# Kernel optimization log

Hardware: AMD Instinct MI355X
Metric: run time of the kernel (lower is better)

The kernel has to match this reference:

```python
import jax, jax.numpy as jnp
import numpy as np

INPUT_DIM = 1024
HIDDEN_DIM = 2048
NUM_BLOCKS = 8
BLOCK_SIZE = HIDDEN_DIM // NUM_BLOCKS
BATCH = 2048


def setup_inputs() -> dict:
    key = jax.random.key(0)
    ks = jax.random.split(key, 6)
    # PyTorch GRUCell init: uniform(-1/sqrt(hidden_size), 1/sqrt(hidden_size))
    bound = 1.0 / np.sqrt(BLOCK_SIZE)
    u = lambda k, shape: jax.random.uniform(k, shape, jnp.float32, -bound, bound)
    return {
        "input": jax.random.normal(ks[0], (BATCH, INPUT_DIM), jnp.float32),
        "hidden": jax.random.normal(ks[1], (BATCH, HIDDEN_DIM), jnp.float32),
        # stacked per-block GRUCell params (block-diagonal structure)
        "W_ih": u(ks[2], (NUM_BLOCKS, 3 * BLOCK_SIZE, INPUT_DIM)),
        "W_hh": u(ks[3], (NUM_BLOCKS, 3 * BLOCK_SIZE, BLOCK_SIZE)),
        "b_ih": u(ks[4], (NUM_BLOCKS, 3 * BLOCK_SIZE)),
        "b_hh": u(ks[5], (NUM_BLOCKS, 3 * BLOCK_SIZE)),
    }


def reference(input, hidden, W_ih, W_hh, b_ih, b_hh):
    B = input.shape[0]
    nb, g3, bs = W_hh.shape  # [num_blocks, 3*block_size, block_size]
    hb = hidden.reshape(B, nb, bs)                      # [B, nb, bs]
    # input-to-gate and hidden-to-gate projections, batched over blocks
    gi = jnp.einsum("bi,ngi->bng", input, W_ih) + b_ih  # [B, nb, 3*bs]
    gh = jnp.einsum("bns,ngs->bng", hb, W_hh) + b_hh    # [B, nb, 3*bs]
    i_r, i_z, i_n = jnp.split(gi, 3, axis=-1)
    h_r, h_z, h_n = jnp.split(gh, 3, axis=-1)
    r = jax.nn.sigmoid(i_r + h_r)
    z = jax.nn.sigmoid(i_z + h_z)
    n = jnp.tanh(i_n + r * h_n)
    new_h = (1.0 - z) * n + z * hb                      # [B, nb, bs]
    return new_h.reshape(B, nb * bs)
```

## Files before the change

### kernel.cpp

```cpp
#include <hip/hip_runtime.h>
#include <hip/hip_bf16.h>
#include <type_traits>

typedef __attribute__((ext_vector_type(4))) float f32x4;
typedef __attribute__((ext_vector_type(8))) short bf16x8;

template <int V> using ic = std::integral_constant<int, V>;

static constexpr int B_   = 2048;
static constexpr int IN_  = 1024;
static constexpr int HID_ = 2048;
static constexpr int NB_  = 8;
static constexpr int BS_  = 256;
static constexpr int G3_  = 768;

__device__ __forceinline__ unsigned cvtpk(float lo, float hi) {
  unsigned r;
  asm("v_cvt_pk_bf16_f32 %0, %1, %2" : "=v"(r) : "v"(lo), "v"(hi));
  return r;
}

__global__ __launch_bounds__(256, 2) void gru_mfma(
    const float* __restrict__ xf,
    const float* __restrict__ hf,
    const float* __restrict__ Wih,
    const float* __restrict__ Whh,
    const float* __restrict__ b_ih,
    const float* __restrict__ b_hh,
    float* __restrict__ out)
{
  __shared__ __align__(16) char lds[2][40960];

  const int t    = threadIdx.x;
  const int lane = t & 63;
  const int wid  = t >> 6;
  const int wm   = wid >> 1;
  const int wn   = wid & 1;

  const int bid = blockIdx.x;
  const int swz = (bid & 7) * 64 + (bid >> 3);
  const int mrow0 = (swz & 15) * 128;
  const int ct    = swz >> 4;
  const int n     = ct >> 2;
  const int s0    = (ct & 3) * 64;

  int arow[4], acol[4];
#pragma unroll
  for (int p = 0; p < 4; ++p) {
    int op = p * 4096 + t * 16;
    int ol = op ^ (((op >> 7) & 7) << 4);
    arow[p] = ol >> 7;
    acol[p] = (ol & 127) >> 1;
  }
  int wgrow[6], wcol[6];
#pragma unroll
  for (int q = 0; q < 6; ++q) {
    int op = q * 4096 + t * 16;
    int ol = op ^ (((op >> 7) & 7) << 4);
    int wr = ol >> 7;
    wgrow[q] = n * G3_ + (wr >> 6) * BS_ + s0 + (wr & 63);
    wcol[q]  = (ol & 127) >> 1;
  }

  f32x4 acc[4][4][2] = {};
  float4 st[4][2];

  auto issueA = [&](int t2) {
#pragma unroll
    for (int p = 0; p < 4; ++p) {
      const float* src = (t2 < 16)
        ? xf + (size_t)(mrow0 + arow[p]) * IN_  + t2 * 64 + acol[p]
        : hf + (size_t)(mrow0 + arow[p]) * HID_ + n * BS_ + (t2 - 16) * 64 + acol[p];
      st[p][0] = *reinterpret_cast<const float4*>(src);
      st[p][1] = *reinterpret_cast<const float4*>(src + 4);
    }
  };
  auto issueW = [&](int t2, int q0) {
#pragma unroll
    for (int j = 0; j < 3; ++j) {
      const int q = q0 + j;
      const float* src = (t2 < 16)
        ? Wih + (size_t)wgrow[q] * IN_ + t2 * 64 + wcol[q]
        : Whh + (size_t)wgrow[q] * BS_ + (t2 - 16) * 64 + wcol[q];
      st[j][0] = *reinterpret_cast<const float4*>(src);
      st[j][1] = *reinterpret_cast<const float4*>(src + 4);
    }
  };
  auto pack8 = [&](const float4& a, const float4& b) {
    union { unsigned u[4]; bf16x8 v; } r;
    r.u[0] = cvtpk(a.x, a.y); r.u[1] = cvtpk(a.z, a.w);
    r.u[2] = cvtpk(b.x, b.y); r.u[3] = cvtpk(b.z, b.w);
    return r.v;
  };
  auto writeA = [&](char* buf) {
#pragma unroll
    for (int p = 0; p < 4; ++p)
      *reinterpret_cast<bf16x8*>(buf + p * 4096 + t * 16) = pack8(st[p][0], st[p][1]);
  };
  auto writeW = [&](char* buf, int q0) {
#pragma unroll
    for (int j = 0; j < 3; ++j)
      *reinterpret_cast<bf16x8*>(buf + 16384 + (q0 + j) * 4096 + t * 16) = pack8(st[j][0], st[j][1]);
  };

  auto loadA = [&](const char* buf, bf16x8 (&af)[2][4]) {
#pragma unroll
    for (int ksub = 0; ksub < 2; ++ksub)
#pragma unroll
      for (int mi = 0; mi < 4; ++mi) {
        int ar  = wm * 64 + mi * 16 + (lane & 15);
        int off = ar * 128 + ksub * 64 + ((lane >> 4) * 16);
        off ^= (ar & 7) << 4;
        af[ksub][mi] = *reinterpret_cast<const bf16x8*>(buf + off);
      }
  };
  auto loadW = [&](const char* buf, int g, bf16x8 (&wf)[2][2]) {
#pragma unroll
    for (int ksub = 0; ksub < 2; ++ksub)
#pragma unroll
      for (int ni = 0; ni < 2; ++ni) {
        int wr  = g * 64 + wn * 32 + ni * 16 + (lane & 15);
        int off = wr * 128 + ksub * 64 + ((lane >> 4) * 16);
        off ^= (wr & 7) << 4;
        wf[ksub][ni] = *reinterpret_cast<const bf16x8*>(buf + 16384 + off);
      }
  };
  auto mfmaSet = [&](auto setc, bf16x8 (&af)[2][4], bf16x8 (&wf)[2][2]) {
    constexpr int set = decltype(setc)::value;
    __builtin_amdgcn_s_setprio(1);
#pragma unroll
    for (int ksub = 0; ksub < 2; ++ksub)
#pragma unroll
      for (int mi = 0; mi < 4; ++mi)
#pragma unroll
        for (int ni = 0; ni < 2; ++ni)
          acc[set][mi][ni] = __builtin_amdgcn_mfma_f32_16x16x32_bf16(
              af[ksub][mi], wf[ksub][ni], acc[set][mi][ni], 0, 0, 0);
    __builtin_amdgcn_s_setprio(0);
  };

  issueA(0);
  writeA((char*)lds[0]);
  issueW(0, 0);
  writeW((char*)lds[0], 0);
  issueW(0, 3);
  writeW((char*)lds[0], 3);
  __syncthreads();

#pragma unroll
  for (int tt = 0; tt < 20; ++tt) {
    char* cur = (char*)lds[tt & 1];
    char* oth = (char*)lds[(tt & 1) ^ 1];
    bf16x8 af[2][4], wf[2][2];

    if (tt < 19) issueA(tt + 1);
    __builtin_amdgcn_sched_barrier(0);
    loadA(cur, af);
    loadW(cur, 0, wf);
    mfmaSet(ic<0>{}, af, wf);
    __builtin_amdgcn_sched_barrier(0);
    if (tt < 19) { writeA(oth); issueW(tt + 1, 0); }
    __builtin_amdgcn_sched_barrier(0);
    loadW(cur, 1, wf);
    mfmaSet(ic<1>{}, af, wf);
    __builtin_amdgcn_sched_barrier(0);
    if (tt < 19) { writeW(oth, 0); issueW(tt + 1, 3); }
    __builtin_amdgcn_sched_barrier(0);
    loadW(cur, 2, wf);
    if (tt < 16) mfmaSet(ic<2>{}, af, wf);
    else         mfmaSet(ic<3>{}, af, wf);
    __builtin_amdgcn_sched_barrier(0);
    if (tt < 19) writeW(oth, 3);
    __syncthreads();
  }

#pragma unroll
  for (int ni = 0; ni < 2; ++ni) {
    int scol = s0 + wn * 32 + ni * 16 + (lane & 15);
    float br_i = b_ih[n * G3_ + 0 * BS_ + scol];
    float bz_i = b_ih[n * G3_ + 1 * BS_ + scol];
    float bn_i = b_ih[n * G3_ + 2 * BS_ + scol];
    float br_h = b_hh[n * G3_ + 0 * BS_ + scol];
    float bz_h = b_hh[n * G3_ + 1 * BS_ + scol];
    float bn_h = b_hh[n * G3_ + 2 * BS_ + scol];
    int gcol = n * BS_ + scol;
#pragma unroll
    for (int mi = 0; mi < 4; ++mi) {
#pragma unroll
      for (int i = 0; i < 4; ++i) {
        int row = mrow0 + wm * 64 + mi * 16 + (lane >> 4) * 4 + i;
        float hprev = hf[(size_t)row * HID_ + gcol];
        float rr = acc[0][mi][ni][i] + br_i + br_h;
        float zz = acc[1][mi][ni][i] + bz_i + bz_h;
        float r  = 1.f / (1.f + __expf(-rr));
        float z  = 1.f / (1.f + __expf(-zz));
        float ng = tanhf(acc[2][mi][ni][i] + bn_i + r * (acc[3][mi][ni][i] + bn_h));
        out[(size_t)row * HID_ + gcol] = (1.f - z) * ng + z * hprev;
      }
    }
  }
}

extern "C" void kernel_launch(void* const* d_in, const int* in_sizes, int n_in,
                              void* d_out, int out_size, void* d_ws, size_t ws_size,
                              hipStream_t stream) {
  const float* x   = (const float*)d_in[0];
  const float* h   = (const float*)d_in[1];
  const float* Wih = (const float*)d_in[2];
  const float* Whh = (const float*)d_in[3];
  const float* bih = (const float*)d_in[4];
  const float* bhh = (const float*)d_in[5];
  float* out = (float*)d_out;
  (void)d_ws; (void)ws_size;

  gru_mfma<<<512, 256, 0, stream>>>(x, h, Wih, Whh, bih, bhh, out);
}
```

Baseline: 53.73 us.

## Halve K-tile to 32 and issue all next-tile loads before compute

Halves the K step per iteration from 64 to 32, so LDS per buffer drops from 40KB to 20KB and the loop runs 40 iterations instead of 20. All global loads for the next tile (A and the three W gates) are now issued together before compute, and their LDS writes happen after the MFMAs. Loads are no longer staggered between gate MFMA sets, and the LDS swizzle is changed to a 4-way XOR for 64-byte rows. The smaller LDS footprint could allow more blocks per CU, but doubling the number of iterations also doubles the barriers, and each MFMA phase is shorter for hiding latency.

```diff
diff --git a/kernel.cpp b/kernel.cpp
--- a/kernel.cpp
+++ b/kernel.cpp
@@ -29,7 +29,7 @@
     const float* __restrict__ b_hh,
     float* __restrict__ out)
 {
-  __shared__ __align__(16) char lds[2][40960];
+  __shared__ __align__(16) char lds[2][20480];
 
   const int t    = threadIdx.x;
   const int lane = t & 63;
@@ -44,46 +44,44 @@
   const int n     = ct >> 2;
   const int s0    = (ct & 3) * 64;
 
-  int arow[4], acol[4];
+  int arow[2], acolE[2];
 #pragma unroll
-  for (int p = 0; p < 4; ++p) {
+  for (int p = 0; p < 2; ++p) {
     int op = p * 4096 + t * 16;
-    int ol = op ^ (((op >> 7) & 7) << 4);
-    arow[p] = ol >> 7;
-    acol[p] = (ol & 127) >> 1;
+    int ol = op ^ (((op >> 6) & 3) << 4);
+    arow[p]  = ol >> 6;
+    acolE[p] = (ol & 63) >> 1;
   }
-  int wgrow[6], wcol[6];
+  int wgrow[3], wcolE[3];
 #pragma unroll
-  for (int q = 0; q < 6; ++q) {
+  for (int q = 0; q < 3; ++q) {
     int op = q * 4096 + t * 16;
-    int ol = op ^ (((op >> 7) & 7) << 4);
-    int wr = ol >> 7;
-    wgrow[q] = n * G3_ + (wr >> 6) * BS_ + s0 + (wr & 63);
-    wcol[q]  = (ol & 127) >> 1;
+    int ol = op ^ (((op >> 6) & 3) << 4);
+    int wr = ol >> 6;
+    wgrow[q]  = n * G3_ + (wr >> 6) * BS_ + s0 + (wr & 63);
+    wcolE[q]  = (ol & 63) >> 1;
   }
 
   f32x4 acc[4][4][2] = {};
-  float4 st[4][2];
+  float4 sa[2][2];
+  float4 sw[3][2];
 
-  auto issueA = [&](int t2) {
+  auto issue = [&](int tt) {
 #pragma unroll
-    for (int p = 0; p < 4; ++p) {
-      const float* src = (t2 < 16)
-        ? xf + (size_t)(mrow0 + arow[p]) * IN_  + t2 * 64 + acol[p]
-        : hf + (size_t)(mrow0 + arow[p]) * HID_ + n * BS_ + (t2 - 16) * 64 + acol[p];
-      st[p][0] = *reinterpret_cast<const float4*>(src);
-      st[p][1] = *reinterpret_cast<const float4*>(src + 4);
+    for (int p = 0; p < 2; ++p) {
+      const float* src = (tt < 32)
+        ? xf + (size_t)(mrow0 + arow[p]) * IN_  + tt * 32 + acolE[p]
+        : hf + (size_t)(mrow0 + arow[p]) * HID_ + n * BS_ + (tt - 32) * 32 + acolE[p];
+      sa[p][0] = *reinterpret_cast<const float4*>(src);
+      sa[p][1] = *reinterpret_cast<const float4*>(src + 4);
     }
-  };
-  auto issueW = [&](int t2, int q0) {
 #pragma unroll
-    for (int j = 0; j < 3; ++j) {
-      const int q = q0 + j;
-      const float* src = (t2 < 16)
-        ? Wih + (size_t)wgrow[q] * IN_ + t2 * 64 + wcol[q]
-        : Whh + (size_t)wgrow[q] * BS_ + (t2 - 16) * 64 + wcol[q];
-      st[j][0] = *reinterpret_cast<const float4*>(src);
-      st[j][1] = *reinterpret_cast<const float4*>(src + 4);
+    for (int q = 0; q < 3; ++q) {
+      const float* src = (tt < 32)
+        ? Wih + (size_t)wgrow[q] * IN_ + tt * 32 + wcolE[q]
+        : Whh + (size_t)wgrow[q] * BS_ + (tt - 32) * 32 + wcolE[q];
+      sw[q][0] = *reinterpret_cast<const float4*>(src);
+      sw[q][1] = *reinterpret_cast<const float4*>(src + 4);
     }
   };
   auto pack8 = [&](const float4& a, const float4& b) {
@@ -92,85 +90,62 @@
     r.u[2] = cvtpk(b.x, b.y); r.u[3] = cvtpk(b.z, b.w);
     return r.v;
   };
-  auto writeA = [&](char* buf) {
+  auto writeAll = [&](int buf) {
+    char* base = (char*)lds[buf];
 #pragma unroll
-    for (int p = 0; p < 4; ++p)
-      *reinterpret_cast<bf16x8*>(buf + p * 4096 + t * 16) = pack8(st[p][0], st[p][1]);
-  };
-  auto writeW = [&](char* buf, int q0) {
+    for (int p = 0; p < 2; ++p)
+      *reinterpret_cast<bf16x8*>(base + p * 4096 + t * 16) = pack8(sa[p][0], sa[p][1]);
 #pragma unroll
-    for (int j = 0; j < 3; ++j)
-      *reinterpret_cast<bf16x8*>(buf + 16384 + (q0 + j) * 4096 + t * 16) = pack8(st[j][0], st[j][1]);
+    for (int q = 0; q < 3; ++q)
+      *reinterpret_cast<bf16x8*>(base + 8192 + q * 4096 + t * 16) = pack8(sw[q][0], sw[q][1]);
   };
 
-  auto loadA = [&](const char* buf, bf16x8 (&af)[2][4]) {
+  auto compute = [&](int buf, auto ph1c) {
+    constexpr bool PH1 = decltype(ph1c)::value;
+    const char* base = (const char*)lds[buf];
+    bf16x8 af[4];
 #pragma unroll
-    for (int ksub = 0; ksub < 2; ++ksub)
+    for (int mi = 0; mi < 4; ++mi) {
+      int ar  = wm * 64 + mi * 16 + (lane & 15);
+      int off = (ar * 64 + ((lane >> 4) * 16)) ^ ((ar & 3) << 4);
+      af[mi] = *reinterpret_cast<const bf16x8*>(base + off);
+    }
+    __builtin_amdgcn_s_setprio(1);
 #pragma unroll
-      for (int mi = 0; mi < 4; ++mi) {
-        int ar  = wm * 64 + mi * 16 + (lane & 15);
-        int off = ar * 128 + ksub * 64 + ((lane >> 4) * 16);
-        off ^= (ar & 7) << 4;
-        af[ksub][mi] = *reinterpret_cast<const bf16x8*>(buf + off);
-      }
-  };
-  auto loadW = [&](const char* buf, int g, bf16x8 (&wf)[2][2]) {
-#pragma unroll
-    for (int ksub = 0; ksub < 2; ++ksub)
+    for (int g = 0; g < 3; ++g) {
+      bf16x8 wf[2];
 #pragma unroll
       for (int ni = 0; ni < 2; ++ni) {
         int wr  = g * 64 + wn * 32 + ni * 16 + (lane & 15);
-        int off = wr * 128 + ksub * 64 + ((lane >> 4) * 16);
-        off ^= (wr & 7) << 4;
-        wf[ksub][ni] = *reinterpret_cast<const bf16x8*>(buf + 16384 + off);
+        int off = (wr * 64 + ((lane >> 4) * 16)) ^ ((wr & 3) << 4);
+        wf[ni] = *reinterpret_cast<const bf16x8*>(base + 8192 + off);
       }
-  };
-  auto mfmaSet = [&](auto setc, bf16x8 (&af)[2][4], bf16x8 (&wf)[2][2]) {
-    constexpr int set = decltype(setc)::value;
-    __builtin_amdgcn_s_setprio(1);
-#pragma unroll
-    for (int ksub = 0; ksub < 2; ++ksub)
+      constexpr int set2 = PH1 ? 2 : 3;
+      const int set = (g < 2) ? g : set2;
 #pragma unroll
       for (int mi = 0; mi < 4; ++mi)
 #pragma unroll
         for (int ni = 0; ni < 2; ++ni)
           acc[set][mi][ni] = __builtin_amdgcn_mfma_f32_16x16x32_bf16(
-              af[ksub][mi], wf[ksub][ni], acc[set][mi][ni], 0, 0, 0);
+              af[mi], wf[ni], acc[set][mi][ni], 0, 0, 0);
+    }
     __builtin_amdgcn_s_setprio(0);
   };
 
-  issueA(0);
-  writeA((char*)lds[0]);
-  issueW(0, 0);
-  writeW((char*)lds[0], 0);
-  issueW(0, 3);
-  writeW((char*)lds[0], 3);
+  issue(0);
+  writeAll(0);
   __syncthreads();
 
 #pragma unroll
-  for (int tt = 0; tt < 20; ++tt) {
-    char* cur = (char*)lds[tt & 1];
-    char* oth = (char*)lds[(tt & 1) ^ 1];
-    bf16x8 af[2][4], wf[2][2];
+  for (int tt = 0; tt < 40; ++tt) {
+    const int cur = tt & 1;
 
-    if (tt < 19) issueA(tt + 1);
+    if (tt < 39) issue(tt + 1);
     __builtin_amdgcn_sched_barrier(0);
-    loadA(cur, af);
-    loadW(cur, 0, wf);
-    mfmaSet(ic<0>{}, af, wf);
+    if (tt < 32) compute(cur, std::true_type{});
+    else         compute(cur, std::false_type{});
     __builtin_amdgcn_sched_barrier(0);
-    if (tt < 19) { writeA(oth); issueW(tt + 1, 0); }
-    __builtin_amdgcn_sched_barrier(0);
-    loadW(cur, 1, wf);
-    mfmaSet(ic<1>{}, af, wf);
-    __builtin_amdgcn_sched_barrier(0);
-    if (tt < 19) { writeW(oth, 0); issueW(tt + 1, 3); }
-    __builtin_amdgcn_sched_barrier(0);
-    loadW(cur, 2, wf);
-    if (tt < 16) mfmaSet(ic<2>{}, af, wf);
-    else         mfmaSet(ic<3>{}, af, wf);
-    __builtin_amdgcn_sched_barrier(0);
-    if (tt < 19) writeW(oth, 3);
+    if (tt < 39) writeAll(cur ^ 1);
     __syncthreads();
   }
 
```

Result: faster. 52.57 us, median of 3 (-2.2%).
